# Performance work log

Measured on AMD Instinct MI355X. Metric: run time of the kernel, lower is better.

The kernel has to match this reference:

```python
import jax, jax.numpy as jnp
import numpy as np
import math

B, S, E, H = 2, 4096, 1024, 16
W = 256  # one-sided attention window (attention_window // 2)


def setup_inputs() -> dict:
    key = jax.random.key(0)
    ks = jax.random.split(key, 7)
    init = lambda k, shp: jax.random.normal(k, shp, jnp.float32) * 0.02
    return {
        "hidden_states": jax.random.normal(ks[0], (B, S, E), jnp.float32),
        "attention_mask": jnp.zeros((B, S), jnp.int32),  # 0 = local attention
        "q_w": init(ks[1], (E, E)), "q_b": jnp.zeros((E,), jnp.float32),
        "k_w": init(ks[2], (E, E)), "k_b": jnp.zeros((E,), jnp.float32),
        "v_w": init(ks[3], (E, E)), "v_b": jnp.zeros((E,), jnp.float32),
    }


def _banded_attention(hidden_states, attention_mask, q_w, q_b, k_w, k_b, v_w, v_b):
    D = E // H          # head dim
    w = W               # one-sided window
    nc = S // w         # number of query chunks of length w
    # Projections (torch Linear: x @ W.T + b); query pre-scaled by sqrt(head_dim)
    q = (hidden_states @ q_w.T + q_b) / math.sqrt(D)
    k = hidden_states @ k_w.T + k_b
    v = hidden_states @ v_w.T + v_b
    heads = lambda x: x.reshape(B, S, H, D).transpose(0, 2, 1, 3)  # [B,H,S,D]
    q, k, v = heads(q), heads(k), heads(v)

    qc = q.reshape(B, H, nc, w, D)                       # [B,H,nc,w,D]
    pad = lambda x: jnp.pad(x, ((0, 0), (0, 0), (w, w), (0, 0)))
    # chunk c of keys/values covers padded positions [c*w, c*w + 3w)
    idx = (jnp.arange(nc) * w)[:, None] + jnp.arange(3 * w)[None, :]  # [nc,3w]
    kc = pad(k)[:, :, idx]                               # [B,H,nc,3w,D]
    vc = pad(v)[:, :, idx]                               # [B,H,nc,3w,D]

    # banded scores: query x in chunk attends padded key y; rel offset = y-w-x
    scores = jnp.einsum('bhcxd,bhcyd->bhcxy', qc, kc)    # [B,H,nc,w,3w]

    # additive mask from attention_mask (!=0 -> -10000 at that key position)
    fm = jnp.where(attention_mask != 0, -10000.0, 0.0)   # [B,S]
    fmc = jnp.pad(fm, ((0, 0), (w, w)))[:, idx]          # [B,nc,3w]
    scores = scores + fmc[:, None, :, None, :]

    # validity: |rel| <= w (the 2w+1 band) and key index j in [0, S)
    x = jnp.arange(w)[:, None]                           # [w,1]
    y = jnp.arange(3 * w)[None, :]                       # [1,3w]
    rel = y - w - x                                      # [w,3w]
    j = (jnp.arange(nc) * w)[:, None, None] + (y - w)[None]  # [nc,1,3w] key idx
    valid = (jnp.abs(rel) <= w)[None] & (j >= 0) & (j < S)   # [nc,w,3w]
    scores = jnp.where(valid[None, None], scores, -jnp.inf)

    probs = jax.nn.softmax(scores.astype(jnp.float32), axis=-1)
    ctx = jnp.einsum('bhcxy,bhcyd->bhcxd', probs, vc)    # [B,H,nc,w,D]
    return ctx.reshape(B, H, S, D).transpose(0, 2, 1, 3).reshape(B, S, E)


def reference(hidden_states, attention_mask, q_w, q_b, k_w, k_b, v_w, v_b):
    return _banded_attention(hidden_states, attention_mask,
                             q_w, q_b, k_w, k_b, v_w, v_b)
```

## Files before the change

kernel.cpp:

```cpp
#include <hip/hip_runtime.h>
#include <math.h>

constexpr int Bn  = 2;
constexpr int Sn  = 4096;
constexpr int En  = 1024;
constexpr int Hn  = 16;
constexpr int Mtot = Bn * Sn;
constexpr int Kp  = 1024;
constexpr int PAD = 72;

typedef __bf16    bf16x8 __attribute__((ext_vector_type(8)));
typedef __bf16    bf16x4 __attribute__((ext_vector_type(4)));
typedef _Float16  f16x8  __attribute__((ext_vector_type(8)));
typedef _Float16  f16x4  __attribute__((ext_vector_type(4)));
typedef float     f32x4  __attribute__((ext_vector_type(4)));

__global__ void __launch_bounds__(256)
cvt_hs_kernel(const float* __restrict__ hs, _Float16* __restrict__ hs16)
{
    int t = blockIdx.x * 256 + threadIdx.x;
    int m = t >> 8;
    int k = (t & 255) << 2;
    float4 x = *(const float4*)&hs[((size_t)m << 10) + k];
    f16x4 h;
    h[0] = (_Float16)x.x; h[1] = (_Float16)x.y;
    h[2] = (_Float16)x.z; h[3] = (_Float16)x.w;
    *(f16x4*)&hs16[((size_t)m << 10) + k] = h;
}

__global__ void __launch_bounds__(256)
cvt_w_kernel(const float* __restrict__ qw, const float* __restrict__ kw,
             const float* __restrict__ vw, _Float16* __restrict__ w16)
{
    int t = blockIdx.x * 256 + threadIdx.x;
    int gn = t >> 8;
    int k  = (t & 255) << 2;
    int p  = gn >> 10, n = gn & 1023;
    const float* src = (p == 0) ? qw : (p == 1) ? kw : vw;
    float4 x = *(const float4*)&src[((size_t)n << 10) + k];
    f16x4 h;
    h[0] = (_Float16)x.x; h[1] = (_Float16)x.y;
    h[2] = (_Float16)x.z; h[3] = (_Float16)x.w;
    *(f16x4*)&w16[((size_t)gn << 10) + k] = h;
}

__device__ inline void load_lds16(const void* g, void* s) {
    __builtin_amdgcn_global_load_lds((const __attribute__((address_space(1))) void*)g,
                                     (__attribute__((address_space(3))) void*)s,
                                     16, 0, 0);
}

__global__ void __launch_bounds__(256)
qkv_mfma_kernel(const _Float16* __restrict__ A2, const _Float16* __restrict__ B2,
                const float* __restrict__ qb, const float* __restrict__ kb,
                const float* __restrict__ vb,
                __bf16* __restrict__ q16, __bf16* __restrict__ k16,
                __bf16* __restrict__ vt16)
{
    __shared__ _Float16 As[128 * 32];
    __shared__ _Float16 Bs[128 * 32];

    const int tid  = threadIdx.x;
    const int m0   = blockIdx.x * 128;
    const int n0   = blockIdx.y * 128;
    const int w    = tid >> 6;
    const int lane = tid & 63;
    const int wm   = w >> 1, wn = w & 1;
    const int mrow = lane & 15, quad = lane >> 4;

    const int stRow = w * 16 + (lane >> 2);
    const int stCol = (lane & 3) * 8;

    f32x4 acc[4][4] = {};

    const _Float16* Abase = A2 + (size_t)(m0 + stRow) * Kp + stCol;
    const _Float16* Bbase = B2 + (size_t)(n0 + stRow) * Kp + stCol;
    _Float16* AsW = &As[w * 512];
    _Float16* BsW = &Bs[w * 512];

    for (int k0 = 0; k0 < Kp; k0 += 32) {
        load_lds16(Abase + k0,            AsW);
        load_lds16(Abase + 64 * Kp + k0,  AsW + 2048);
        load_lds16(Bbase + k0,            BsW);
        load_lds16(Bbase + 64 * Kp + k0,  BsW + 2048);
        __syncthreads();
        f16x8 af[4], bfr[4];
#pragma unroll
        for (int t = 0; t < 4; t++) {
            af[t]  = *(const f16x8*)&As[(wm * 64 + t * 16 + mrow) * 32 + quad * 8];
            bfr[t] = *(const f16x8*)&Bs[(wn * 64 + t * 16 + mrow) * 32 + quad * 8];
        }
#pragma unroll
        for (int ti = 0; ti < 4; ti++)
#pragma unroll
            for (int tj = 0; tj < 4; tj++)
                acc[ti][tj] = __builtin_amdgcn_mfma_f32_16x16x32_f16(
                    af[ti], bfr[tj], acc[ti][tj], 0, 0, 0);
        __syncthreads();
    }

    const int p = n0 >> 10;
    const float* bptr = (p == 0) ? qb : (p == 1) ? kb : vb;
#pragma unroll
    for (int tj = 0; tj < 4; tj++) {
        const int n  = n0 + wn * 64 + tj * 16 + mrow;
        const float bv = bptr[n & 1023];
        const int hh = (n & 1023) >> 6, dd = n & 63;
#pragma unroll
        for (int ti = 0; ti < 4; ti++) {
            const int m  = m0 + wm * 64 + ti * 16 + quad * 4;
            const int bb = m >> 12, ss = m & 4095;
            const size_t bhh = (size_t)(bb * Hn + hh);
            if (p == 0) {
#pragma unroll
                for (int r = 0; r < 4; r++)
                    q16[(bhh * Sn + ss + r) * 64 + dd] =
                        (__bf16)((acc[ti][tj][r] + bv) * 0.125f);
            } else if (p == 1) {
#pragma unroll
                for (int r = 0; r < 4; r++)
                    k16[(bhh * Sn + ss + r) * 64 + dd] =
                        (__bf16)(acc[ti][tj][r] + bv);
            } else {
                bf16x4 pv4;
#pragma unroll
                for (int r = 0; r < 4; r++)
                    pv4[r] = (__bf16)(acc[ti][tj][r] + bv);
                *(bf16x4*)&vt16[(bhh * 64 + dd) * (size_t)Sn + ss] = pv4;
            }
        }
    }
}

__global__ void __launch_bounds__(256, 2)
banded_attn_kernel(const __bf16* __restrict__ q16, const __bf16* __restrict__ k16,
                   const __bf16* __restrict__ vt16, const int* __restrict__ mask,
                   float* __restrict__ out)
{
    __shared__ __bf16 Kt[2][64 * PAD];
    __shared__ __bf16 Vt[2][64 * PAD];
    __shared__ __bf16 Pt[4][64 * PAD];
    __shared__ float  Msh[768];

    const int c = blockIdx.x, h = blockIdx.y, b = blockIdx.z;
    const int bh = b * Hn + h;
    const int i0 = c * 256;
    const int jwin0 = i0 - 256;
    const int tid  = threadIdx.x;
    const int wv   = tid >> 6;
    const int lane = tid & 63;
    const int quad = lane >> 4, mrow = lane & 15;

#pragma unroll
    for (int rep = 0; rep < 3; rep++) {
        int idx = rep * 256 + tid;
        int jg  = jwin0 + idx;
        float mv = 0.f;
        if (jg >= 0 && jg < Sn && mask[b * Sn + jg] != 0) mv = -10000.f;
        Msh[idx] = mv;
    }

    bf16x8 qf[4][2];
    const __bf16* qbase = q16 + (((size_t)bh * Sn + i0 + wv * 64) << 6);
#pragma unroll
    for (int tjq = 0; tjq < 4; tjq++)
#pragma unroll
        for (int kc = 0; kc < 2; kc++)
            qf[tjq][kc] = *(const bf16x8*)(qbase + (16 * tjq + mrow) * 64 + 32 * kc + 8 * quad);

    const int sr = lane >> 3;
    const int sc = lane & 7;
    bf16x8 kreg0, kreg1, vreg0, vreg1;
    auto gload = [&](int st) {
        const int j0 = jwin0 + st * 64;
        const int r0 = wv * 16 + sr;
        const int r1 = wv * 16 + 8 + sr;
        int jk0 = j0 + r0; jk0 = jk0 < 0 ? 0 : (jk0 > Sn - 1 ? Sn - 1 : jk0);
        int jk1 = j0 + r1; jk1 = jk1 < 0 ? 0 : (jk1 > Sn - 1 ? Sn - 1 : jk1);
        kreg0 = *(const bf16x8*)&k16[(((size_t)bh * Sn + jk0) << 6) + sc * 8];
        kreg1 = *(const bf16x8*)&k16[(((size_t)bh * Sn + jk1) << 6) + sc * 8];
        int jv = j0 + sc * 8; jv = jv < 0 ? 0 : (jv > Sn - 8 ? Sn - 8 : jv);
        vreg0 = *(const bf16x8*)&vt16[((size_t)bh * 64 + r0) * Sn + jv];
        vreg1 = *(const bf16x8*)&vt16[((size_t)bh * 64 + r1) * Sn + jv];
    };
    auto swrite = [&](int buf) {
        *(bf16x8*)&Kt[buf][(wv * 16 + sr) * PAD + sc * 8]     = kreg0;
        *(bf16x8*)&Kt[buf][(wv * 16 + 8 + sr) * PAD + sc * 8] = kreg1;
        *(bf16x8*)&Vt[buf][(wv * 16 + sr) * PAD + sc * 8]     = vreg0;
        *(bf16x8*)&Vt[buf][(wv * 16 + 8 + sr) * PAD + sc * 8] = vreg1;
    };

    f32x4 acc_o[4][4] = {};
    float lrun[4] = {0.f, 0.f, 0.f, 0.f};
    __bf16* Pw = &Pt[wv][0];

    gload(0);
    swrite(0);
    __syncthreads();

    for (int st = 0; st < 12; st++) {
        const int buf = st & 1;
        if (st + 1 < 12) gload(st + 1);

        if (st >= wv && st <= wv + 8) {
            const __bf16* KtB = &Kt[buf][0];
            const __bf16* VtB = &Vt[buf][0];
#pragma unroll
            for (int ti = 0; ti < 4; ti++) {
                bf16x8 ak0 = *(const bf16x8*)&KtB[(16 * ti + mrow) * PAD + quad * 8];
                bf16x8 ak1 = *(const bf16x8*)&KtB[(16 * ti + mrow) * PAD + 32 + quad * 8];
                const int y0 = 64 * st + 16 * ti + 4 * quad;
                f32x4 ms4 = *(const f32x4*)&Msh[y0];
#pragma unroll
                for (int tjq = 0; tjq < 4; tjq++) {
                    f32x4 s = {};
                    s = __builtin_amdgcn_mfma_f32_16x16x32_bf16(ak0, qf[tjq][0], s, 0, 0, 0);
                    s = __builtin_amdgcn_mfma_f32_16x16x32_bf16(ak1, qf[tjq][1], s, 0, 0, 0);
                    const int xq = 64 * wv + 16 * tjq + mrow;
                    bf16x4 pk;
                    float psum = 0.f;
#pragma unroll
                    for (int r = 0; r < 4; r++) {
                        const int y = y0 + r;
                        bool ok = ((unsigned)(y - xq) <= 512u) &
                                  ((unsigned)(jwin0 + y) < 4096u);
                        float pv = ok ? __expf(s[r] + ms4[r]) : 0.f;
                        psum += pv;
                        pk[r] = (__bf16)pv;
                    }
                    lrun[tjq] += psum;
                    *(bf16x4*)&Pw[(16 * tjq + mrow) * PAD + 16 * ti + 4 * quad] = pk;
                }
            }
#pragma unroll
            for (int kc2 = 0; kc2 < 2; kc2++) {
                bf16x8 av[4];
#pragma unroll
                for (int dt = 0; dt < 4; dt++)
                    av[dt] = *(const bf16x8*)&VtB[(16 * dt + mrow) * PAD + kc2 * 32 + quad * 8];
#pragma unroll
                for (int tjq = 0; tjq < 4; tjq++) {
                    bf16x8 pf = *(const bf16x8*)&Pw[(16 * tjq + mrow) * PAD + kc2 * 32 + quad * 8];
#pragma unroll
                    for (int dt = 0; dt < 4; dt++)
                        acc_o[dt][tjq] = __builtin_amdgcn_mfma_f32_16x16x32_bf16(
                            av[dt], pf, acc_o[dt][tjq], 0, 0, 0);
                }
            }
        }

        if (st + 1 < 12) {
            swrite((st + 1) & 1);
            __syncthreads();
        }
    }

    float inv[4];
#pragma unroll
    for (int tjq = 0; tjq < 4; tjq++) {
        float l = lrun[tjq];
        l += __shfl_xor(l, 16);
        l += __shfl_xor(l, 32);
        inv[tjq] = 1.0f / l;
    }
#pragma unroll
    for (int dt = 0; dt < 4; dt++)
#pragma unroll
        for (int tjq = 0; tjq < 4; tjq++) {
            f32x4 o = acc_o[dt][tjq];
            o[0] *= inv[tjq]; o[1] *= inv[tjq]; o[2] *= inv[tjq]; o[3] *= inv[tjq];
            float* dst = out + ((size_t)(b * Sn + i0 + wv * 64 + 16 * tjq + mrow)) * En
                             + h * 64 + 16 * dt + 4 * quad;
            *(f32x4*)dst = o;
        }
}

extern "C" void kernel_launch(void* const* d_in, const int* in_sizes, int n_in,
                              void* d_out, int out_size, void* d_ws, size_t ws_size,
                              hipStream_t stream) {
    const float* hs  = (const float*)d_in[0];
    const int*  mask = (const int*)d_in[1];
    const float* qw  = (const float*)d_in[2];
    const float* qb  = (const float*)d_in[3];
    const float* kw  = (const float*)d_in[4];
    const float* kb  = (const float*)d_in[5];
    const float* vw  = (const float*)d_in[6];
    const float* vb  = (const float*)d_in[7];
    float* out = (float*)d_out;

    _Float16* hs16 = (_Float16*)d_ws;
    _Float16* w16  = (_Float16*)((char*)d_ws + (size_t)16777216);
    __bf16*   q16  = (__bf16*)((char*)d_ws + (size_t)23068672);
    __bf16*   k16  = (__bf16*)((char*)d_ws + (size_t)39845888);
    __bf16*   vt16 = (__bf16*)((char*)d_ws + (size_t)56623104);

    cvt_hs_kernel<<<8192, 256, 0, stream>>>(hs, hs16);
    cvt_w_kernel <<<3072, 256, 0, stream>>>(qw, kw, vw, w16);

    dim3 pgrid(Mtot / 128, 3072 / 128);
    qkv_mfma_kernel<<<pgrid, 256, 0, stream>>>(hs16, w16, qb, kb, vb, q16, k16, vt16);

    dim3 agrid(Sn / 256, Hn, Bn);
    banded_attn_kernel<<<agrid, 256, 0, stream>>>(q16, k16, vt16, mask, out);
}
```

Baseline: 216.4 us.

## Halve attention query tile, single-buffer K/V, skip masks on interior stages

```diff
diff --git a/kernel.cpp b/kernel.cpp
--- a/kernel.cpp
+++ b/kernel.cpp
@@ -7,7 +7,10 @@
 constexpr int Hn  = 16;
 constexpr int Mtot = Bn * Sn;
 constexpr int Kp  = 1024;
-constexpr int PAD = 72;
+constexpr int QT   = 128;
+constexpr int NST  = 10;
+constexpr int PADK = 68;
+constexpr int PADP = 36;
 
 typedef __bf16    bf16x8 __attribute__((ext_vector_type(8)));
 typedef __bf16    bf16x4 __attribute__((ext_vector_type(4)));
@@ -132,19 +135,19 @@
     }
 }
 
-__global__ void __launch_bounds__(256, 2)
+__global__ void __launch_bounds__(256, 4)
 banded_attn_kernel(const __bf16* __restrict__ q16, const __bf16* __restrict__ k16,
                    const __bf16* __restrict__ vt16, const int* __restrict__ mask,
                    float* __restrict__ out)
 {
-    __shared__ __bf16 Kt[2][64 * PAD];
-    __shared__ __bf16 Vt[2][64 * PAD];
-    __shared__ __bf16 Pt[4][64 * PAD];
-    __shared__ float  Msh[768];
+    __shared__ __bf16 Kt[64 * PADK];
+    __shared__ __bf16 Vt[64 * PADK];
+    __shared__ __bf16 Pt[4][32 * PADP];
+    __shared__ float  Msh[704];
 
     const int c = blockIdx.x, h = blockIdx.y, b = blockIdx.z;
     const int bh = b * Hn + h;
-    const int i0 = c * 256;
+    const int i0 = c * QT;
     const int jwin0 = i0 - 256;
     const int tid  = threadIdx.x;
     const int wv   = tid >> 6;
@@ -154,16 +157,18 @@
 #pragma unroll
     for (int rep = 0; rep < 3; rep++) {
         int idx = rep * 256 + tid;
-        int jg  = jwin0 + idx;
-        float mv = 0.f;
-        if (jg >= 0 && jg < Sn && mask[b * Sn + jg] != 0) mv = -10000.f;
-        Msh[idx] = mv;
-    }
-
-    bf16x8 qf[4][2];
-    const __bf16* qbase = q16 + (((size_t)bh * Sn + i0 + wv * 64) << 6);
-#pragma unroll
-    for (int tjq = 0; tjq < 4; tjq++)
+        if (idx < 640) {
+            int jg = jwin0 + idx;
+            float mv = 0.f;
+            if (jg >= 0 && jg < Sn && mask[b * Sn + jg] != 0) mv = -10000.f;
+            Msh[idx] = mv;
+        }
+    }
+
+    bf16x8 qf[2][2];
+    const __bf16* qbase = q16 + (((size_t)bh * Sn + i0 + wv * 32) << 6);
+#pragma unroll
+    for (int tjq = 0; tjq < 2; tjq++)
 #pragma unroll
         for (int kc = 0; kc < 2; kc++)
             qf[tjq][kc] = *(const bf16x8*)(qbase + (16 * tjq + mrow) * 64 + 32 * kc + 8 * quad);
@@ -183,64 +188,77 @@
         vreg0 = *(const bf16x8*)&vt16[((size_t)bh * 64 + r0) * Sn + jv];
         vreg1 = *(const bf16x8*)&vt16[((size_t)bh * 64 + r1) * Sn + jv];
     };
-    auto swrite = [&](int buf) {
-        *(bf16x8*)&Kt[buf][(wv * 16 + sr) * PAD + sc * 8]     = kreg0;
-        *(bf16x8*)&Kt[buf][(wv * 16 + 8 + sr) * PAD + sc * 8] = kreg1;
-        *(bf16x8*)&Vt[buf][(wv * 16 + sr) * PAD + sc * 8]     = vreg0;
-        *(bf16x8*)&Vt[buf][(wv * 16 + 8 + sr) * PAD + sc * 8] = vreg1;
+    auto swrite = [&]() {
+        *(bf16x8*)&Kt[(wv * 16 + sr) * PADK + sc * 8]     = kreg0;
+        *(bf16x8*)&Kt[(wv * 16 + 8 + sr) * PADK + sc * 8] = kreg1;
+        *(bf16x8*)&Vt[(wv * 16 + sr) * PADK + sc * 8]     = vreg0;
+        *(bf16x8*)&Vt[(wv * 16 + 8 + sr) * PADK + sc * 8] = vreg1;
     };
 
-    f32x4 acc_o[4][4] = {};
-    float lrun[4] = {0.f, 0.f, 0.f, 0.f};
+    f32x4 acc_o[4][2] = {};
+    float lrun[2] = {0.f, 0.f};
     __bf16* Pw = &Pt[wv][0];
+    const int stlo = wv >> 1;
 
     gload(0);
-    swrite(0);
-    __syncthreads();
-
-    for (int st = 0; st < 12; st++) {
-        const int buf = st & 1;
-        if (st + 1 < 12) gload(st + 1);
-
-        if (st >= wv && st <= wv + 8) {
-            const __bf16* KtB = &Kt[buf][0];
-            const __bf16* VtB = &Vt[buf][0];
-#pragma unroll
-            for (int ti = 0; ti < 4; ti++) {
-                bf16x8 ak0 = *(const bf16x8*)&KtB[(16 * ti + mrow) * PAD + quad * 8];
-                bf16x8 ak1 = *(const bf16x8*)&KtB[(16 * ti + mrow) * PAD + 32 + quad * 8];
-                const int y0 = 64 * st + 16 * ti + 4 * quad;
-                f32x4 ms4 = *(const f32x4*)&Msh[y0];
-#pragma unroll
-                for (int tjq = 0; tjq < 4; tjq++) {
-                    f32x4 s = {};
-                    s = __builtin_amdgcn_mfma_f32_16x16x32_bf16(ak0, qf[tjq][0], s, 0, 0, 0);
-                    s = __builtin_amdgcn_mfma_f32_16x16x32_bf16(ak1, qf[tjq][1], s, 0, 0, 0);
-                    const int xq = 64 * wv + 16 * tjq + mrow;
-                    bf16x4 pk;
-                    float psum = 0.f;
-#pragma unroll
-                    for (int r = 0; r < 4; r++) {
-                        const int y = y0 + r;
-                        bool ok = ((unsigned)(y - xq) <= 512u) &
-                                  ((unsigned)(jwin0 + y) < 4096u);
-                        float pv = ok ? __expf(s[r] + ms4[r]) : 0.f;
-                        psum += pv;
-                        pk[r] = (__bf16)pv;
+    for (int st = 0; st < NST; st++) {
+        __syncthreads();
+        swrite();
+        __syncthreads();
+        if (st + 1 < NST) gload(st + 1);
+
+        const int j0 = jwin0 + 64 * st;
+        const bool activ = (st >= stlo) && (st <= stlo + 8) &&
+                           (j0 + 63 >= 0) && (j0 < Sn);
+        if (activ) {
+            const bool fast = (st > stlo) && (st < stlo + 8) &&
+                              (j0 >= 0) && (j0 + 63 < Sn);
+#pragma unroll
+            for (int half = 0; half < 2; half++) {
+#pragma unroll
+                for (int t2 = 0; t2 < 2; t2++) {
+                    const int ti = 2 * half + t2;
+                    bf16x8 ak0 = *(const bf16x8*)&Kt[(16 * ti + mrow) * PADK + quad * 8];
+                    bf16x8 ak1 = *(const bf16x8*)&Kt[(16 * ti + mrow) * PADK + 32 + quad * 8];
+                    const int y0 = 64 * st + 16 * ti + 4 * quad;
+                    f32x4 ms4 = *(const f32x4*)&Msh[y0];
+#pragma unroll
+                    for (int tjq = 0; tjq < 2; tjq++) {
+                        f32x4 s = {};
+                        s = __builtin_amdgcn_mfma_f32_16x16x32_bf16(ak0, qf[tjq][0], s, 0, 0, 0);
+                        s = __builtin_amdgcn_mfma_f32_16x16x32_bf16(ak1, qf[tjq][1], s, 0, 0, 0);
+                        bf16x4 pk;
+                        float psum = 0.f;
+                        if (fast) {
+#pragma unroll
+                            for (int r = 0; r < 4; r++) {
+                                float pv = __expf(s[r] + ms4[r]);
+                                psum += pv;
+                                pk[r] = (__bf16)pv;
+                            }
+                        } else {
+                            const int xq = 32 * wv + 16 * tjq + mrow;
+#pragma unroll
+                            for (int r = 0; r < 4; r++) {
+                                const int y = y0 + r;
+                                bool ok = ((unsigned)(y - xq) <= 512u) &
+                                          ((unsigned)(jwin0 + y) < 4096u);
+                                float pv = ok ? __expf(s[r] + ms4[r]) : 0.f;
+                                psum += pv;
+                                pk[r] = (__bf16)pv;
+                            }
+                        }
+                        lrun[tjq] += psum;
+                        *(bf16x4*)&Pw[(16 * tjq + mrow) * PADP + 16 * t2 + 4 * quad] = pk;
                     }
-                    lrun[tjq] += psum;
-                    *(bf16x4*)&Pw[(16 * tjq + mrow) * PAD + 16 * ti + 4 * quad] = pk;
                 }
-            }
-#pragma unroll
-            for (int kc2 = 0; kc2 < 2; kc2++) {
                 bf16x8 av[4];
 #pragma unroll
                 for (int dt = 0; dt < 4; dt++)
-                    av[dt] = *(const bf16x8*)&VtB[(16 * dt + mrow) * PAD + kc2 * 32 + quad * 8];
-#pragma unroll
-                for (int tjq = 0; tjq < 4; tjq++) {
-                    bf16x8 pf = *(const bf16x8*)&Pw[(16 * tjq + mrow) * PAD + kc2 * 32 + quad * 8];
+                    av[dt] = *(const bf16x8*)&Vt[(16 * dt + mrow) * PADK + 32 * half + quad * 8];
+#pragma unroll
+                for (int tjq = 0; tjq < 2; tjq++) {
+                    bf16x8 pf = *(const bf16x8*)&Pw[(16 * tjq + mrow) * PADP + quad * 8];
 #pragma unroll
                     for (int dt = 0; dt < 4; dt++)
                         acc_o[dt][tjq] = __builtin_amdgcn_mfma_f32_16x16x32_bf16(
@@ -248,16 +266,11 @@
                 }
             }
         }
-
-        if (st + 1 < 12) {
-            swrite((st + 1) & 1);
-            __syncthreads();
-        }
-    }
-
-    float inv[4];
-#pragma unroll
-    for (int tjq = 0; tjq < 4; tjq++) {
+    }
+
+    float inv[2];
+#pragma unroll
+    for (int tjq = 0; tjq < 2; tjq++) {
         float l = lrun[tjq];
         l += __shfl_xor(l, 16);
         l += __shfl_xor(l, 32);
@@ -266,10 +279,10 @@
 #pragma unroll
     for (int dt = 0; dt < 4; dt++)
 #pragma unroll
-        for (int tjq = 0; tjq < 4; tjq++) {
+        for (int tjq = 0; tjq < 2; tjq++) {
             f32x4 o = acc_o[dt][tjq];
             o[0] *= inv[tjq]; o[1] *= inv[tjq]; o[2] *= inv[tjq]; o[3] *= inv[tjq];
-            float* dst = out + ((size_t)(b * Sn + i0 + wv * 64 + 16 * tjq + mrow)) * En
+            float* dst = out + ((size_t)(b * Sn + i0 + wv * 32 + 16 * tjq + mrow)) * En
                              + h * 64 + 16 * dt + 4 * quad;
             *(f32x4*)dst = o;
         }
@@ -300,6 +313,6 @@
     dim3 pgrid(Mtot / 128, 3072 / 128);
     qkv_mfma_kernel<<<pgrid, 256, 0, stream>>>(hs16, w16, qb, kb, vb, q16, k16, vt16);
 
-    dim3 agrid(Sn / 256, Hn, Bn);
+    dim3 agrid(Sn / QT, Hn, Bn);
     banded_attn_kernel<<<agrid, 256, 0, stream>>>(q16, k16, vt16, mask, out);
 }
```

Measured after the change: 221.6 us. 2.4% more time.
